# Optimization experiments

Measured on AMD Instinct MI355X. Metric: run time of the kernel, lower is better.

## Reference

```python
import jax, jax.numpy as jnp
import numpy as np

N_NODES = 50000
IN_DIM = 128
HIDDEN = 64
OUT_DIM = 3
HEADS1 = 4
NEG_SLOPE = 0.2
EPS = 1e-16


def _glorot(key, shape):
    fan_in, fan_out = shape[0], shape[-1]
    lim = (6.0 / (fan_in + fan_out)) ** 0.5
    return jax.random.uniform(key, shape, jnp.float32, -lim, lim)


def setup_inputs() -> dict:
    key = jax.random.key(0)
    ks = jax.random.split(key, 12)
    x = jax.random.normal(ks[0], (N_NODES, IN_DIM), jnp.float32)
    edge_index = jax.random.randint(ks[1], (2, 400000), 0, N_NODES, jnp.int64)
    # layer 1: GATConv(in=128, out=64, heads=4)
    W1 = _glorot(ks[2], (IN_DIM, HEADS1 * HIDDEN))
    att_src1 = _glorot(ks[3], (HEADS1, HIDDEN))
    att_dst1 = _glorot(ks[4], (HEADS1, HIDDEN))
    b1 = jnp.zeros((HEADS1 * HIDDEN,), jnp.float32)
    # layer 2: GATConv(in=256, out=64, heads=1)
    W2 = _glorot(ks[5], (HEADS1 * HIDDEN, HIDDEN))
    att_src2 = _glorot(ks[6], (1, HIDDEN))
    att_dst2 = _glorot(ks[7], (1, HIDDEN))
    b2 = jnp.zeros((HIDDEN,), jnp.float32)
    # output linear
    Wout = _glorot(ks[8], (HIDDEN, OUT_DIM))
    bout = jnp.zeros((OUT_DIM,), jnp.float32)
    return {"x": x, "edge_index": edge_index, "W1": W1, "att_src1": att_src1,
            "att_dst1": att_dst1, "b1": b1, "W2": W2, "att_src2": att_src2,
            "att_dst2": att_dst2, "b2": b2, "Wout": Wout, "bout": bout}


def gat_conv(x, src, dst, W, a_src, a_dst, b, n_nodes):
    H, C = a_src.shape
    h = (x @ W).reshape(n_nodes, H, C)            # [N,H,C]
    a_s = jnp.sum(h * a_src[None], axis=-1)        # [N,H]
    a_d = jnp.sum(h * a_dst[None], axis=-1)        # [N,H]
    e = jax.nn.leaky_relu(a_s[src] + a_d[dst], NEG_SLOPE)  # [E,H]
    # segment softmax over incoming edges of each dst node
    m = jax.ops.segment_max(e, dst, num_segments=n_nodes)
    ex = jnp.exp(e - m[dst])
    denom = jax.ops.segment_sum(ex, dst, num_segments=n_nodes)
    alpha = ex / (denom[dst] + EPS)                # [E,H]
    msg = h[src] * alpha[..., None]                # [E,H,C]
    out = jax.ops.segment_sum(msg, dst, num_segments=n_nodes)
    return out.reshape(n_nodes, H * C) + b


def reference(x, edge_index, W1, att_src1, att_dst1, b1, W2, att_src2, att_dst2, b2, Wout, bout):
    n = x.shape[0]
    loop = jnp.arange(n, dtype=edge_index.dtype)
    src = jnp.concatenate([edge_index[0], loop])   # add self loops (PyG default)
    dst = jnp.concatenate([edge_index[1], loop])
    h = gat_conv(x, src, dst, W1, att_src1, att_dst1, b1, n)
    h = jax.nn.elu(h)
    h = gat_conv(h, src, dst, W2, att_src2, att_dst2, b2, n)
    h = jax.nn.elu(h)
    return h @ Wout + bout
```

## Files before the change

kernel.cpp:

```cpp
#include <hip/hip_runtime.h>
#include <hip/hip_bf16.h>
#include <math.h>

#define N_NODES  50000
#define IN_DIM   128
#define HIDDEN   64
#define OUT_DIM  3
#define HEADS1   4
#define E_RAW    400000
#define E_TOT    450000
#define NEG_SLOPE 0.2f
#define N_CHUNKS 49
#define WPREP_BLOCKS 128
#define EB_SC ((E_TOT + 255) / 256)
#define MB_GE (N_NODES / 16)

typedef __attribute__((ext_vector_type(8))) short bf16x8;
typedef __attribute__((ext_vector_type(4))) float f32x4;

static __device__ __forceinline__ float bfu(unsigned short u) {
    return __uint_as_float(((unsigned)u) << 16);
}
static __device__ __forceinline__ unsigned short f2b_bits(float v) {
    __hip_bfloat16 b = __float2bfloat16(v);
    return *reinterpret_cast<unsigned short*>(&b);
}

static __device__ __forceinline__ void get_edge(const int* __restrict__ ei, int is64,
                                                int e, int& s, int& d) {
    if (e >= E_RAW) { s = d = e - E_RAW; return; }
    if (is64) { s = ei[2 * e]; d = ei[2 * E_RAW + 2 * e]; }
    else      { s = ei[e];     d = ei[E_RAW + e]; }
    s = min(max(s, 0), N_NODES - 1);
    d = min(max(d, 0), N_NODES - 1);
}

static __device__ __forceinline__ int block_is64(const int* __restrict__ ei,
                                                 int e, bool valid, int* nzbuf) {
    bool real = valid && (e < E_RAW);
    int hv = real ? ei[2 * e + 1] : 0;
    if (threadIdx.x == 0) *nzbuf = 0;
    __syncthreads();
    if (__any(hv != 0) && (threadIdx.x & 63) == 0) *nzbuf = 1;
    __syncthreads();
    return (*nzbuf == 0);
}

__global__ void wprep_count_kernel(const float* __restrict__ W1, __hip_bfloat16* __restrict__ W1T,
                                   const float* __restrict__ W2, __hip_bfloat16* __restrict__ W2T,
                                   const int* __restrict__ ei, int* __restrict__ deg) {
    __shared__ int nz;
    int bid = blockIdx.x;
    if (bid < WPREP_BLOCKS) {
        int i = bid * 256 + threadIdx.x;
        if (i < 256 * 128) {
            int n = i >> 7, k = i & 127;
            *((unsigned short*)W1T + i) = f2b_bits(W1[k * 256 + n]);
        }
        if (i < 64 * 256) {
            int n = i >> 8, k = i & 255;
            *((unsigned short*)W2T + i) = f2b_bits(W2[k * 64 + n]);
        }
        return;
    }
    int e = (bid - WPREP_BLOCKS) * 256 + threadIdx.x;
    bool valid = e < E_TOT;
    int is64 = block_is64(ei, e, valid, &nz);
    if (!valid) return;
    int s, d;
    get_edge(ei, is64, e, s, d);
    atomicAdd(&deg[d], 1);
}

__global__ void scan_fused_kernel(const int* __restrict__ deg, int* __restrict__ row_ptr,
                                  int* __restrict__ cursor) {
    __shared__ int wsum[4];
    __shared__ int sbase;
    const int bid = blockIdx.x, t = threadIdx.x, wv = t >> 6, ln = t & 63;
    int base = 0;
    const int ng = bid * 256;
    for (int g = t; g < ng; g += 256) {
        int4 d = ((const int4*)deg)[g];
        base += (d.x + d.y) + (d.z + d.w);
    }
    #pragma unroll
    for (int off = 1; off < 64; off <<= 1) base += __shfl_xor(base, off, 64);
    if (ln == 0) wsum[wv] = base;
    __syncthreads();
    if (t == 0) sbase = wsum[0] + wsum[1] + wsum[2] + wsum[3];
    __syncthreads();
    base = sbase;
    int g = bid * 256 + t;
    int4 d = (g < 12500) ? ((const int4*)deg)[g] : make_int4(0, 0, 0, 0);
    int p0 = d.x, p1 = p0 + d.y, p2 = p1 + d.z, p3 = p2 + d.w;
    int s = p3;
    #pragma unroll
    for (int off = 1; off < 64; off <<= 1) {
        int u = __shfl_up(s, off, 64);
        if (ln >= off) s += u;
    }
    if (ln == 63) wsum[wv] = s;
    __syncthreads();
    int wbase = base;
    #pragma unroll
    for (int w = 0; w < 4; w++) wbase += (w < wv) ? wsum[w] : 0;
    int ex = wbase + s - p3;
    if (g < 12500) {
        int i = g * 4;
        row_ptr[i + 1] = ex + p0; row_ptr[i + 2] = ex + p1;
        row_ptr[i + 3] = ex + p2; row_ptr[i + 4] = ex + p3;
        cursor[i]     = ex;       cursor[i + 1]  = ex + p0;
        cursor[i + 2] = ex + p1;  cursor[i + 3]  = ex + p2;
    }
    if (bid == 0 && t == 0) row_ptr[0] = 0;
}

__global__ void __launch_bounds__(256) scatter_gemm_l1_kernel(
        const int* __restrict__ ei,
        int* __restrict__ cursor, int* __restrict__ csr_src,
        const float* __restrict__ x, const __hip_bfloat16* __restrict__ W1T,
        const float* __restrict__ att_s, const float* __restrict__ att_d,
        __hip_bfloat16* __restrict__ h1,
        float* __restrict__ asb4, float* __restrict__ adb4) {
    __shared__ unsigned short As[16][136];
    __shared__ __attribute__((aligned(16))) unsigned short hT[16][264];
    __shared__ int nz;
    if (blockIdx.x < EB_SC) {
        int e = blockIdx.x * 256 + threadIdx.x;
        bool valid = e < E_TOT;
        int is64 = block_is64(ei, e, valid, &nz);
        if (!valid) return;
        int s, d;
        get_edge(ei, is64, e, s, d);
        int pos = atomicAdd(&cursor[d], 1);
        csr_src[pos] = s;
        return;
    }
    const int tid = threadIdx.x;
    const int wave = tid >> 6, lane = tid & 63;
    const int quad = lane >> 4, m = lane & 15;
    const int row0 = (blockIdx.x - EB_SC) * 16;
    {
        int r = tid >> 4, seg = tid & 15;
        const float* xa = x + (size_t)(row0 + r) * IN_DIM + seg * 8;
        float4 u = *(const float4*)xa;
        float4 v = *(const float4*)(xa + 4);
        ushort4 p0, p1;
        p0.x = f2b_bits(u.x); p0.y = f2b_bits(u.y); p0.z = f2b_bits(u.z); p0.w = f2b_bits(u.w);
        p1.x = f2b_bits(v.x); p1.y = f2b_bits(v.y); p1.z = f2b_bits(v.z); p1.w = f2b_bits(v.w);
        *(ushort4*)&As[r][seg * 8]     = p0;
        *(ushort4*)&As[r][seg * 8 + 4] = p1;
    }
    __syncthreads();
    const int n0w = wave * 64;
    f32x4 acc0 = {0.f, 0.f, 0.f, 0.f}, acc1 = acc0, acc2 = acc0, acc3 = acc0;
    #pragma unroll
    for (int k0 = 0; k0 < IN_DIM; k0 += 32) {
        int kk = k0 + quad * 8;
        bf16x8 a = *(const bf16x8*)&As[m][kk];
        bf16x8 b0 = *(const bf16x8*)(W1T + (size_t)(n0w +  0 + m) * IN_DIM + kk);
        bf16x8 b1 = *(const bf16x8*)(W1T + (size_t)(n0w + 16 + m) * IN_DIM + kk);
        bf16x8 b2 = *(const bf16x8*)(W1T + (size_t)(n0w + 32 + m) * IN_DIM + kk);
        bf16x8 b3 = *(const bf16x8*)(W1T + (size_t)(n0w + 48 + m) * IN_DIM + kk);
        acc0 = __builtin_amdgcn_mfma_f32_16x16x32_bf16(a, b0, acc0, 0, 0, 0);
        acc1 = __builtin_amdgcn_mfma_f32_16x16x32_bf16(a, b1, acc1, 0, 0, 0);
        acc2 = __builtin_amdgcn_mfma_f32_16x16x32_bf16(a, b2, acc2, 0, 0, 0);
        acc3 = __builtin_amdgcn_mfma_f32_16x16x32_bf16(a, b3, acc3, 0, 0, 0);
    }
    float ats0 = att_s[n0w +  0 + m], atd0 = att_d[n0w +  0 + m];
    float ats1 = att_s[n0w + 16 + m], atd1 = att_d[n0w + 16 + m];
    float ats2 = att_s[n0w + 32 + m], atd2 = att_d[n0w + 32 + m];
    float ats3 = att_s[n0w + 48 + m], atd3 = att_d[n0w + 48 + m];
    #pragma unroll
    for (int i = 0; i < 4; i++) {
        int r = quad * 4 + i;
        hT[r][n0w +  0 + m] = f2b_bits(acc0[i]);
        hT[r][n0w + 16 + m] = f2b_bits(acc1[i]);
        hT[r][n0w + 32 + m] = f2b_bits(acc2[i]);
        hT[r][n0w + 48 + m] = f2b_bits(acc3[i]);
        float ps = acc0[i] * ats0 + acc1[i] * ats1 + acc2[i] * ats2 + acc3[i] * ats3;
        float pd = acc0[i] * atd0 + acc1[i] * atd1 + acc2[i] * atd2 + acc3[i] * atd3;
        #pragma unroll
        for (int off = 1; off < 16; off <<= 1) {
            ps += __shfl_xor(ps, off, 16);
            pd += __shfl_xor(pd, off, 16);
        }
        if (m == 0) {
            asb4[(row0 + r) * 4 + wave] = ps;
            adb4[(row0 + r) * 4 + wave] = pd;
        }
    }
    __syncthreads();
    {
        unsigned short* hrow = (unsigned short*)h1;
        int r0 = tid >> 5, c0 = tid & 31;
        *(bf16x8*)(hrow + (size_t)(row0 + r0) * 256 + c0 * 8) = *(const bf16x8*)&hT[r0][c0 * 8];
        int S = tid + 256;
        int r1 = S >> 5, c1 = S & 31;
        *(bf16x8*)(hrow + (size_t)(row0 + r1) * 256 + c1 * 8) = *(const bf16x8*)&hT[r1][c1 * 8];
    }
}

__global__ void __launch_bounds__(1024, 8) gat_gather4_l2_kernel(
        const int* __restrict__ row_ptr, const int* __restrict__ csr_src,
        const float* __restrict__ asb4, const float* __restrict__ adb4,
        const __hip_bfloat16* __restrict__ h1, const float* __restrict__ bias,
        const __hip_bfloat16* __restrict__ W2T,
        const float* __restrict__ att_s, const float* __restrict__ att_d,
        __hip_bfloat16* __restrict__ h2,
        float* __restrict__ asb, float* __restrict__ adb) {
    __shared__ __attribute__((aligned(16))) unsigned short As[16][264];
    __shared__ __attribute__((aligned(16))) unsigned short hT2[16][72];
    __shared__ float sPS[4][16];
    __shared__ float sPD[4][16];
    const int tid = threadIdx.x;
    const int wave = tid >> 6, lane = tid & 63;
    const int row0 = blockIdx.x * 16;
    const int c    = lane & 31;
    const int slot = lane >> 5;
    const int head = c >> 3;
    const int eidx0 = lane >> 2;
    const int hh   = lane & 3;

    {
        const int n = row0 + wave;
        int b = row_ptr[n], e = row_ptr[n + 1];
        float adnh = adb4[n * 4 + hh];
        float acc[8];
        #pragma unroll
        for (int i = 0; i < 8; i++) acc[i] = 0.f;
        float l = 0.f;
        for (int c0 = b; c0 < e; c0 += 16) {
            int cnt = min(16, e - c0);
            int s_all = (lane < cnt) ? csr_src[c0 + lane] : 0;
            int sE = __shfl(s_all, eidx0, 64);
            float w_all = 0.f;
            if (eidx0 < cnt) {
                float v = asb4[sE * 4 + hh] + adnh;
                v = (v > 0.f) ? v : NEG_SLOPE * v;
                w_all = __expf(v);
            }
            #pragma unroll 2
            for (int k = 0; k < cnt; k += 2) {
                int eidx = k + slot;
                int s = __shfl(s_all, eidx, 64);
                float w = __shfl(w_all, eidx * 4 + head, 64);
                bf16x8 f = *(const bf16x8*)(h1 + (size_t)s * 256 + c * 8);
                l += w;
                #pragma unroll
                for (int i = 0; i < 8; i++)
                    acc[i] += w * bfu((unsigned short)f[i]);
            }
        }
        #pragma unroll
        for (int i = 0; i < 8; i++) acc[i] += __shfl_xor(acc[i], 32, 64);
        l += __shfl_xor(l, 32, 64);
        if (lane < 32) {
            float il = 1.f / (l + 1e-16f);
            float4 b0 = *(const float4*)(bias + c * 8);
            float4 b1 = *(const float4*)(bias + c * 8 + 4);
            float r[8];
            r[0] = acc[0] * il + b0.x; r[1] = acc[1] * il + b0.y;
            r[2] = acc[2] * il + b0.z; r[3] = acc[3] * il + b0.w;
            r[4] = acc[4] * il + b1.x; r[5] = acc[5] * il + b1.y;
            r[6] = acc[6] * il + b1.z; r[7] = acc[7] * il + b1.w;
            bf16x8 st;
            #pragma unroll
            for (int i = 0; i < 8; i++) {
                float v = (r[i] > 0.f) ? r[i] : expm1f(r[i]);
                st[i] = (short)f2b_bits(v);
            }
            *(bf16x8*)&As[wave][c * 8] = st;
        }
    }
    __syncthreads();

    if (wave < 4) {
        const int quad = lane >> 4, m = lane & 15;
        const int n0 = wave * 16;
        f32x4 acc = {0.f, 0.f, 0.f, 0.f};
        #pragma unroll
        for (int k0 = 0; k0 < 256; k0 += 32) {
            int kk = k0 + quad * 8;
            bf16x8 a = *(const bf16x8*)&As[m][kk];
            bf16x8 bfr = *(const bf16x8*)(W2T + (size_t)(n0 + m) * 256 + kk);
            acc = __builtin_amdgcn_mfma_f32_16x16x32_bf16(a, bfr, acc, 0, 0, 0);
        }
        float ats = att_s[n0 + m], atd = att_d[n0 + m];
        #pragma unroll
        for (int i = 0; i < 4; i++) {
            int r = quad * 4 + i;
            hT2[r][n0 + m] = f2b_bits(acc[i]);
            float ps = acc[i] * ats;
            float pd = acc[i] * atd;
            #pragma unroll
            for (int off = 1; off < 16; off <<= 1) {
                ps += __shfl_xor(ps, off, 16);
                pd += __shfl_xor(pd, off, 16);
            }
            if (m == 0) {
                sPS[wave][r] = ps;
                sPD[wave][r] = pd;
            }
        }
    }
    __syncthreads();
    if (tid < 128) {
        int r = tid >> 3, cs = tid & 7;
        *(bf16x8*)((unsigned short*)h2 + (size_t)(row0 + r) * 64 + cs * 8) =
            *(const bf16x8*)&hT2[r][cs * 8];
    }
    if (tid < 16) {
        float ps = sPS[0][tid] + sPS[1][tid] + sPS[2][tid] + sPS[3][tid];
        float pd = sPD[0][tid] + sPD[1][tid] + sPD[2][tid] + sPD[3][tid];
        asb[row0 + tid] = ps;
        adb[row0 + tid] = pd;
    }
}

__global__ void __launch_bounds__(256) gat_gather1_out_kernel(
        const int* __restrict__ row_ptr, const int* __restrict__ csr_src,
        const float* __restrict__ asb, const float* __restrict__ adb,
        const __hip_bfloat16* __restrict__ h2, const float* __restrict__ bias,
        const float* __restrict__ Wout, const float* __restrict__ bout,
        float* __restrict__ out) {
    int wave = threadIdx.x >> 6;
    int lane = threadIdx.x & 63;
    int n = blockIdx.x * 4 + wave;
    if (n >= N_NODES) return;
    int b = row_ptr[n], e = row_ptr[n + 1];
    const int c    = lane & 7;
    const int slot = lane >> 3;
    float adn = adb[n];
    float acc[8];
    #pragma unroll
    for (int i = 0; i < 8; i++) acc[i] = 0.f;
    float l = 0.f;
    for (int c0 = b; c0 < e; c0 += 64) {
        int cnt = min(64, e - c0);
        int s_all = (lane < cnt) ? csr_src[c0 + lane] : 0;
        float w_all = 0.f;
        if (lane < cnt) {
            float v = asb[s_all] + adn;
            v = (v > 0.f) ? v : NEG_SLOPE * v;
            w_all = __expf(v);
        }
        #pragma unroll 2
        for (int k = 0; k < cnt; k += 8) {
            int eidx = k + slot;
            int s = __shfl(s_all, eidx, 64);
            float w = __shfl(w_all, eidx, 64);
            bf16x8 f = *(const bf16x8*)(h2 + (size_t)s * 64 + c * 8);
            l += w;
            #pragma unroll
            for (int i = 0; i < 8; i++)
                acc[i] += w * bfu((unsigned short)f[i]);
        }
    }
    #pragma unroll
    for (int off = 8; off < 64; off <<= 1) {
        #pragma unroll
        for (int i = 0; i < 8; i++) acc[i] += __shfl_xor(acc[i], off, 64);
        l += __shfl_xor(l, off, 64);
    }
    float il = 1.f / (l + 1e-16f);
    float4 b0 = *(const float4*)(bias + c * 8);
    float4 b1 = *(const float4*)(bias + c * 8 + 4);
    float v[8];
    v[0] = acc[0] * il + b0.x; v[1] = acc[1] * il + b0.y;
    v[2] = acc[2] * il + b0.z; v[3] = acc[3] * il + b0.w;
    v[4] = acc[4] * il + b1.x; v[5] = acc[5] * il + b1.y;
    v[6] = acc[6] * il + b1.z; v[7] = acc[7] * il + b1.w;
    #pragma unroll
    for (int i = 0; i < 8; i++) v[i] = (v[i] > 0.f) ? v[i] : expm1f(v[i]);
    const float* wp = Wout + c * 24;
    float o0 = 0.f, o1 = 0.f, o2 = 0.f;
    #pragma unroll
    for (int i = 0; i < 8; i++) {
        o0 += v[i] * wp[i * 3 + 0];
        o1 += v[i] * wp[i * 3 + 1];
        o2 += v[i] * wp[i * 3 + 2];
    }
    #pragma unroll
    for (int off = 1; off < 8; off <<= 1) {
        o0 += __shfl_xor(o0, off, 64);
        o1 += __shfl_xor(o1, off, 64);
        o2 += __shfl_xor(o2, off, 64);
    }
    if (lane == 0) {
        out[n * OUT_DIM + 0] = o0 + bout[0];
        out[n * OUT_DIM + 1] = o1 + bout[1];
        out[n * OUT_DIM + 2] = o2 + bout[2];
    }
}

extern "C" void kernel_launch(void* const* d_in, const int* in_sizes, int n_in,
                              void* d_out, int out_size, void* d_ws, size_t ws_size,
                              hipStream_t stream) {
    const float* x    = (const float*)d_in[0];
    const int*   ei   = (const int*)d_in[1];
    const float* W1   = (const float*)d_in[2];
    const float* as1  = (const float*)d_in[3];
    const float* ad1  = (const float*)d_in[4];
    const float* b1   = (const float*)d_in[5];
    const float* W2   = (const float*)d_in[6];
    const float* as2  = (const float*)d_in[7];
    const float* ad2  = (const float*)d_in[8];
    const float* b2v  = (const float*)d_in[9];
    const float* Wout = (const float*)d_in[10];
    const float* bout = (const float*)d_in[11];
    float* out = (float*)d_out;

    float* ws    = (float*)d_ws;
    float* asb4  = ws + 16;
    float* adb4  = asb4 + (size_t)N_NODES * 4;
    float* asb1  = adb4 + (size_t)N_NODES * 4;
    float* adb1  = asb1 + N_NODES;
    __hip_bfloat16* h1     = (__hip_bfloat16*)(adb1 + N_NODES);
    __hip_bfloat16* h2     = (__hip_bfloat16*)(h1 + (size_t)N_NODES * 256);
    __hip_bfloat16* W1T    = (__hip_bfloat16*)(h2 + (size_t)N_NODES * 64);
    __hip_bfloat16* W2T    = W1T + 256 * 128;
    int* deg     = (int*)(W2T + 64 * 256);
    int* row_ptr = deg + N_NODES;
    int* cursor  = row_ptr + N_NODES + 16;
    int* csr_src = cursor + N_NODES;

    const int EB = EB_SC;
    const int AB = (N_NODES + 3) / 4;

    hipMemsetAsync(deg, 0, (size_t)N_NODES * sizeof(int), stream);
    wprep_count_kernel<<<WPREP_BLOCKS + EB, 256, 0, stream>>>(W1, W1T, W2, W2T, ei, deg);
    scan_fused_kernel<<<N_CHUNKS, 256, 0, stream>>>(deg, row_ptr, cursor);

    scatter_gemm_l1_kernel<<<EB + MB_GE, 256, 0, stream>>>(ei, cursor, csr_src,
                                                           x, W1T, as1, ad1, h1, asb4, adb4);

    gat_gather4_l2_kernel<<<MB_GE, 1024, 0, stream>>>(row_ptr, csr_src, asb4, adb4, h1, b1,
                                                      W2T, as2, ad2, h2, asb1, adb1);

    gat_gather1_out_kernel<<<AB, 256, 0, stream>>>(row_ptr, csr_src, asb1, adb1, h2,
                                                   b2v, Wout, bout, out);
}
```

Baseline: 260.9 us.

## Fuse GAT pipeline into single persistent cooperative kernel with grid syncs

Replaces the memset plus five separate kernel launches with one cooperative persistent kernel that runs each stage (weight prep, degree count, scan, CSR scatter with layer-1 GEMM, layer-2 gather/GEMM, final gather/output) in grid-stride loops separated by grid.sync. The int64 detection becomes a single vote in block 0 written to a flag, instead of a per-block vote. The aim is to remove launch overhead and inter-kernel gaps. In exchange, every stage is limited to the grid size chosen from occupancy, and the layer-2 stage shrinks from 1024-thread blocks to 256-thread blocks, which may lower parallelism and lengthen the serialized phases.

Result: slower. 726.7 us (+178.6%).

```diff
diff --git a/kernel.cpp b/kernel.cpp
--- a/kernel.cpp
+++ b/kernel.cpp
@@ -1,6 +1,9 @@
 #include <hip/hip_runtime.h>
+#include <hip/hip_cooperative_groups.h>
 #include <hip/hip_bf16.h>
 #include <math.h>
+
+namespace cg = cooperative_groups;
 
 #define N_NODES  50000
 #define IN_DIM   128
@@ -11,9 +14,9 @@
 #define E_TOT    450000
 #define NEG_SLOPE 0.2f
 #define N_CHUNKS 49
-#define WPREP_BLOCKS 128
 #define EB_SC ((E_TOT + 255) / 256)
 #define MB_GE (N_NODES / 16)
+#define AB_G  ((N_NODES + 3) / 4)
 
 typedef __attribute__((ext_vector_type(8))) short bf16x8;
 typedef __attribute__((ext_vector_type(4))) float f32x4;
@@ -35,262 +38,261 @@
     d = min(max(d, 0), N_NODES - 1);
 }
 
-static __device__ __forceinline__ int block_is64(const int* __restrict__ ei,
-                                                 int e, bool valid, int* nzbuf) {
-    bool real = valid && (e < E_RAW);
-    int hv = real ? ei[2 * e + 1] : 0;
-    if (threadIdx.x == 0) *nzbuf = 0;
-    __syncthreads();
-    if (__any(hv != 0) && (threadIdx.x & 63) == 0) *nzbuf = 1;
-    __syncthreads();
-    return (*nzbuf == 0);
-}
-
-__global__ void wprep_count_kernel(const float* __restrict__ W1, __hip_bfloat16* __restrict__ W1T,
-                                   const float* __restrict__ W2, __hip_bfloat16* __restrict__ W2T,
-                                   const int* __restrict__ ei, int* __restrict__ deg) {
-    __shared__ int nz;
-    int bid = blockIdx.x;
-    if (bid < WPREP_BLOCKS) {
-        int i = bid * 256 + threadIdx.x;
-        if (i < 256 * 128) {
-            int n = i >> 7, k = i & 127;
-            *((unsigned short*)W1T + i) = f2b_bits(W1[k * 256 + n]);
-        }
-        if (i < 64 * 256) {
-            int n = i >> 8, k = i & 255;
-            *((unsigned short*)W2T + i) = f2b_bits(W2[k * 64 + n]);
-        }
-        return;
-    }
-    int e = (bid - WPREP_BLOCKS) * 256 + threadIdx.x;
-    bool valid = e < E_TOT;
-    int is64 = block_is64(ei, e, valid, &nz);
-    if (!valid) return;
-    int s, d;
-    get_edge(ei, is64, e, s, d);
-    atomicAdd(&deg[d], 1);
-}
-
-__global__ void scan_fused_kernel(const int* __restrict__ deg, int* __restrict__ row_ptr,
-                                  int* __restrict__ cursor) {
+struct MegaArgs {
+    const float* x; const int* ei;
+    const float* W1; const float* as1; const float* ad1; const float* b1;
+    const float* W2; const float* as2; const float* ad2; const float* b2v;
+    const float* Wout; const float* bout;
+    float* out;
+    int* flag;
+    float *asb4, *adb4, *asb1, *adb1;
+    __hip_bfloat16 *h1, *eluagg, *h2, *W1T, *W2T;
+    int *deg, *row_ptr, *cursor, *csr_src;
+};
+
+__global__ void __launch_bounds__(256) gat_mega_kernel(MegaArgs a) {
+    cg::grid_group grid = cg::this_grid();
+    const int tid = threadIdx.x;
+    const int nb = gridDim.x;
+    const int gsz = nb * 256;
+    const int gid0 = blockIdx.x * 256 + tid;
+    const int wave = tid >> 6, lane = tid & 63;
+
+    __shared__ unsigned short As[16][136];
+    __shared__ __attribute__((aligned(16))) unsigned short hT[16][264];
+    __shared__ float sPS[4][16];
+    __shared__ float sPD[4][16];
+    __shared__ int ivote;
     __shared__ int wsum[4];
     __shared__ int sbase;
-    const int bid = blockIdx.x, t = threadIdx.x, wv = t >> 6, ln = t & 63;
-    int base = 0;
-    const int ng = bid * 256;
-    for (int g = t; g < ng; g += 256) {
-        int4 d = ((const int4*)deg)[g];
-        base += (d.x + d.y) + (d.z + d.w);
-    }
-    #pragma unroll
-    for (int off = 1; off < 64; off <<= 1) base += __shfl_xor(base, off, 64);
-    if (ln == 0) wsum[wv] = base;
-    __syncthreads();
-    if (t == 0) sbase = wsum[0] + wsum[1] + wsum[2] + wsum[3];
-    __syncthreads();
-    base = sbase;
-    int g = bid * 256 + t;
-    int4 d = (g < 12500) ? ((const int4*)deg)[g] : make_int4(0, 0, 0, 0);
-    int p0 = d.x, p1 = p0 + d.y, p2 = p1 + d.z, p3 = p2 + d.w;
-    int s = p3;
-    #pragma unroll
-    for (int off = 1; off < 64; off <<= 1) {
-        int u = __shfl_up(s, off, 64);
-        if (ln >= off) s += u;
-    }
-    if (ln == 63) wsum[wv] = s;
-    __syncthreads();
-    int wbase = base;
-    #pragma unroll
-    for (int w = 0; w < 4; w++) wbase += (w < wv) ? wsum[w] : 0;
-    int ex = wbase + s - p3;
-    if (g < 12500) {
-        int i = g * 4;
-        row_ptr[i + 1] = ex + p0; row_ptr[i + 2] = ex + p1;
-        row_ptr[i + 3] = ex + p2; row_ptr[i + 4] = ex + p3;
-        cursor[i]     = ex;       cursor[i + 1]  = ex + p0;
-        cursor[i + 2] = ex + p1;  cursor[i + 3]  = ex + p2;
-    }
-    if (bid == 0 && t == 0) row_ptr[0] = 0;
-}
-
-__global__ void __launch_bounds__(256) scatter_gemm_l1_kernel(
-        const int* __restrict__ ei,
-        int* __restrict__ cursor, int* __restrict__ csr_src,
-        const float* __restrict__ x, const __hip_bfloat16* __restrict__ W1T,
-        const float* __restrict__ att_s, const float* __restrict__ att_d,
-        __hip_bfloat16* __restrict__ h1,
-        float* __restrict__ asb4, float* __restrict__ adb4) {
-    __shared__ unsigned short As[16][136];
-    __shared__ __attribute__((aligned(16))) unsigned short hT[16][264];
-    __shared__ int nz;
-    if (blockIdx.x < EB_SC) {
-        int e = blockIdx.x * 256 + threadIdx.x;
-        bool valid = e < E_TOT;
-        int is64 = block_is64(ei, e, valid, &nz);
-        if (!valid) return;
+
+    for (int i = gid0; i < N_NODES; i += gsz) a.deg[i] = 0;
+    for (int i = gid0; i < 256 * 128; i += gsz) {
+        int n = i >> 7, k = i & 127;
+        *((unsigned short*)a.W1T + i) = f2b_bits(a.W1[k * 256 + n]);
+    }
+    for (int i = gid0; i < 64 * 256; i += gsz) {
+        int n = i >> 8, k = i & 255;
+        *((unsigned short*)a.W2T + i) = f2b_bits(a.W2[k * 64 + n]);
+    }
+    if (blockIdx.x == 0) {
+        int nzv = 0;
+        #pragma unroll 4
+        for (int t = 0; t < 32; t++) {
+            int i = t * 256 + tid;
+            nzv |= a.ei[2 * i + 1];
+        }
+        if (tid == 0) ivote = 0;
+        __syncthreads();
+        if (__any(nzv != 0) && (tid & 63) == 0) ivote = 1;
+        __syncthreads();
+        if (tid == 0) a.flag[0] = (ivote == 0) ? 1 : 0;
+    }
+    grid.sync();
+
+    const int is64 = a.flag[0];
+    for (int e = gid0; e < E_TOT; e += gsz) {
         int s, d;
-        get_edge(ei, is64, e, s, d);
-        int pos = atomicAdd(&cursor[d], 1);
-        csr_src[pos] = s;
-        return;
-    }
-    const int tid = threadIdx.x;
-    const int wave = tid >> 6, lane = tid & 63;
-    const int quad = lane >> 4, m = lane & 15;
-    const int row0 = (blockIdx.x - EB_SC) * 16;
+        get_edge(a.ei, is64, e, s, d);
+        atomicAdd(&a.deg[d], 1);
+    }
+    grid.sync();
+
+    if (blockIdx.x < N_CHUNKS) {
+        const int bid = blockIdx.x, wv = wave, ln = lane;
+        int base = 0;
+        const int ng = bid * 256;
+        for (int g = tid; g < ng; g += 256) {
+            int4 d = ((const int4*)a.deg)[g];
+            base += (d.x + d.y) + (d.z + d.w);
+        }
+        #pragma unroll
+        for (int off = 1; off < 64; off <<= 1) base += __shfl_xor(base, off, 64);
+        if (ln == 0) wsum[wv] = base;
+        __syncthreads();
+        if (tid == 0) sbase = wsum[0] + wsum[1] + wsum[2] + wsum[3];
+        __syncthreads();
+        base = sbase;
+        int g = bid * 256 + tid;
+        int4 d = (g < 12500) ? ((const int4*)a.deg)[g] : make_int4(0, 0, 0, 0);
+        int p0 = d.x, p1 = p0 + d.y, p2 = p1 + d.z, p3 = p2 + d.w;
+        int s = p3;
+        #pragma unroll
+        for (int off = 1; off < 64; off <<= 1) {
+            int u = __shfl_up(s, off, 64);
+            if (ln >= off) s += u;
+        }
+        if (ln == 63) wsum[wv] = s;
+        __syncthreads();
+        int wbase = base;
+        #pragma unroll
+        for (int w = 0; w < 4; w++) wbase += (w < wv) ? wsum[w] : 0;
+        int ex = wbase + s - p3;
+        if (g < 12500) {
+            int i = g * 4;
+            a.row_ptr[i + 1] = ex + p0; a.row_ptr[i + 2] = ex + p1;
+            a.row_ptr[i + 3] = ex + p2; a.row_ptr[i + 4] = ex + p3;
+            a.cursor[i]     = ex;       a.cursor[i + 1]  = ex + p0;
+            a.cursor[i + 2] = ex + p1;  a.cursor[i + 3]  = ex + p2;
+        }
+        if (bid == 0 && tid == 0) a.row_ptr[0] = 0;
+    }
+    grid.sync();
+
+    for (int vb = blockIdx.x; vb < EB_SC + MB_GE; vb += nb) {
+        if (vb < EB_SC) {
+            int e = vb * 256 + tid;
+            if (e < E_TOT) {
+                int s, d;
+                get_edge(a.ei, is64, e, s, d);
+                int pos = atomicAdd(&a.cursor[d], 1);
+                a.csr_src[pos] = s;
+            }
+        } else {
+            const int quad = lane >> 4, m = lane & 15;
+            const int row0 = (vb - EB_SC) * 16;
+            {
+                int r = tid >> 4, seg = tid & 15;
+                const float* xa = a.x + (size_t)(row0 + r) * IN_DIM + seg * 8;
+                float4 u = *(const float4*)xa;
+                float4 v = *(const float4*)(xa + 4);
+                ushort4 p0, p1;
+                p0.x = f2b_bits(u.x); p0.y = f2b_bits(u.y); p0.z = f2b_bits(u.z); p0.w = f2b_bits(u.w);
+                p1.x = f2b_bits(v.x); p1.y = f2b_bits(v.y); p1.z = f2b_bits(v.z); p1.w = f2b_bits(v.w);
+                *(ushort4*)&As[r][seg * 8]     = p0;
+                *(ushort4*)&As[r][seg * 8 + 4] = p1;
+            }
+            __syncthreads();
+            const int n0w = wave * 64;
+            f32x4 acc0 = {0.f, 0.f, 0.f, 0.f}, acc1 = acc0, acc2 = acc0, acc3 = acc0;
+            #pragma unroll
+            for (int k0 = 0; k0 < IN_DIM; k0 += 32) {
+                int kk = k0 + quad * 8;
+                bf16x8 av = *(const bf16x8*)&As[m][kk];
+                bf16x8 b0 = *(const bf16x8*)(a.W1T + (size_t)(n0w +  0 + m) * IN_DIM + kk);
+                bf16x8 b1 = *(const bf16x8*)(a.W1T + (size_t)(n0w + 16 + m) * IN_DIM + kk);
+                bf16x8 b2 = *(const bf16x8*)(a.W1T + (size_t)(n0w + 32 + m) * IN_DIM + kk);
+                bf16x8 b3 = *(const bf16x8*)(a.W1T + (size_t)(n0w + 48 + m) * IN_DIM + kk);
+                acc0 = __builtin_amdgcn_mfma_f32_16x16x32_bf16(av, b0, acc0, 0, 0, 0);
+                acc1 = __builtin_amdgcn_mfma_f32_16x16x32_bf16(av, b1, acc1, 0, 0, 0);
+                acc2 = __builtin_amdgcn_mfma_f32_16x16x32_bf16(av, b2, acc2, 0, 0, 0);
+                acc3 = __builtin_amdgcn_mfma_f32_16x16x32_bf16(av, b3, acc3, 0, 0, 0);
+            }
+            float ats0 = a.as1[n0w +  0 + m], atd0 = a.ad1[n0w +  0 + m];
+            float ats1 = a.as1[n0w + 16 + m], atd1 = a.ad1[n0w + 16 + m];
+            float ats2 = a.as1[n0w + 32 + m], atd2 = a.ad1[n0w + 32 + m];
+            float ats3 = a.as1[n0w + 48 + m], atd3 = a.ad1[n0w + 48 + m];
+            #pragma unroll
+            for (int i = 0; i < 4; i++) {
+                int r = quad * 4 + i;
+                hT[r][n0w +  0 + m] = f2b_bits(acc0[i]);
+                hT[r][n0w + 16 + m] = f2b_bits(acc1[i]);
+                hT[r][n0w + 32 + m] = f2b_bits(acc2[i]);
+                hT[r][n0w + 48 + m] = f2b_bits(acc3[i]);
+                float ps = acc0[i] * ats0 + acc1[i] * ats1 + acc2[i] * ats2 + acc3[i] * ats3;
+                float pd = acc0[i] * atd0 + acc1[i] * atd1 + acc2[i] * atd2 + acc3[i] * atd3;
+                #pragma unroll
+                for (int off = 1; off < 16; off <<= 1) {
+                    ps += __shfl_xor(ps, off, 16);
+                    pd += __shfl_xor(pd, off, 16);
+                }
+                if (m == 0) {
+                    a.asb4[(row0 + r) * 4 + wave] = ps;
+                    a.adb4[(row0 + r) * 4 + wave] = pd;
+                }
+            }
+            __syncthreads();
+            {
+                unsigned short* hrow = (unsigned short*)a.h1;
+                int r0 = tid >> 5, c0 = tid & 31;
+                *(bf16x8*)(hrow + (size_t)(row0 + r0) * 256 + c0 * 8) = *(const bf16x8*)&hT[r0][c0 * 8];
+                int S = tid + 256;
+                int r1 = S >> 5, c1 = S & 31;
+                *(bf16x8*)(hrow + (size_t)(row0 + r1) * 256 + c1 * 8) = *(const bf16x8*)&hT[r1][c1 * 8];
+            }
+            __syncthreads();
+        }
+    }
+    grid.sync();
+
     {
-        int r = tid >> 4, seg = tid & 15;
-        const float* xa = x + (size_t)(row0 + r) * IN_DIM + seg * 8;
-        float4 u = *(const float4*)xa;
-        float4 v = *(const float4*)(xa + 4);
-        ushort4 p0, p1;
-        p0.x = f2b_bits(u.x); p0.y = f2b_bits(u.y); p0.z = f2b_bits(u.z); p0.w = f2b_bits(u.w);
-        p1.x = f2b_bits(v.x); p1.y = f2b_bits(v.y); p1.z = f2b_bits(v.z); p1.w = f2b_bits(v.w);
-        *(ushort4*)&As[r][seg * 8]     = p0;
-        *(ushort4*)&As[r][seg * 8 + 4] = p1;
-    }
-    __syncthreads();
-    const int n0w = wave * 64;
-    f32x4 acc0 = {0.f, 0.f, 0.f, 0.f}, acc1 = acc0, acc2 = acc0, acc3 = acc0;
-    #pragma unroll
-    for (int k0 = 0; k0 < IN_DIM; k0 += 32) {
-        int kk = k0 + quad * 8;
-        bf16x8 a = *(const bf16x8*)&As[m][kk];
-        bf16x8 b0 = *(const bf16x8*)(W1T + (size_t)(n0w +  0 + m) * IN_DIM + kk);
-        bf16x8 b1 = *(const bf16x8*)(W1T + (size_t)(n0w + 16 + m) * IN_DIM + kk);
-        bf16x8 b2 = *(const bf16x8*)(W1T + (size_t)(n0w + 32 + m) * IN_DIM + kk);
-        bf16x8 b3 = *(const bf16x8*)(W1T + (size_t)(n0w + 48 + m) * IN_DIM + kk);
-        acc0 = __builtin_amdgcn_mfma_f32_16x16x32_bf16(a, b0, acc0, 0, 0, 0);
-        acc1 = __builtin_amdgcn_mfma_f32_16x16x32_bf16(a, b1, acc1, 0, 0, 0);
-        acc2 = __builtin_amdgcn_mfma_f32_16x16x32_bf16(a, b2, acc2, 0, 0, 0);
-        acc3 = __builtin_amdgcn_mfma_f32_16x16x32_bf16(a, b3, acc3, 0, 0, 0);
-    }
-    float ats0 = att_s[n0w +  0 + m], atd0 = att_d[n0w +  0 + m];
-    float ats1 = att_s[n0w + 16 + m], atd1 = att_d[n0w + 16 + m];
-    float ats2 = att_s[n0w + 32 + m], atd2 = att_d[n0w + 32 + m];
-    float ats3 = att_s[n0w + 48 + m], atd3 = att_d[n0w + 48 + m];
-    #pragma unroll
-    for (int i = 0; i < 4; i++) {
-        int r = quad * 4 + i;
-        hT[r][n0w +  0 + m] = f2b_bits(acc0[i]);
-        hT[r][n0w + 16 + m] = f2b_bits(acc1[i]);
-        hT[r][n0w + 32 + m] = f2b_bits(acc2[i]);
-        hT[r][n0w + 48 + m] = f2b_bits(acc3[i]);
-        float ps = acc0[i] * ats0 + acc1[i] * ats1 + acc2[i] * ats2 + acc3[i] * ats3;
-        float pd = acc0[i] * atd0 + acc1[i] * atd1 + acc2[i] * atd2 + acc3[i] * atd3;
-        #pragma unroll
-        for (int off = 1; off < 16; off <<= 1) {
-            ps += __shfl_xor(ps, off, 16);
-            pd += __shfl_xor(pd, off, 16);
-        }
-        if (m == 0) {
-            asb4[(row0 + r) * 4 + wave] = ps;
-            adb4[(row0 + r) * 4 + wave] = pd;
-        }
-    }
-    __syncthreads();
-    {
-        unsigned short* hrow = (unsigned short*)h1;
-        int r0 = tid >> 5, c0 = tid & 31;
-        *(bf16x8*)(hrow + (size_t)(row0 + r0) * 256 + c0 * 8) = *(const bf16x8*)&hT[r0][c0 * 8];
-        int S = tid + 256;
-        int r1 = S >> 5, c1 = S & 31;
-        *(bf16x8*)(hrow + (size_t)(row0 + r1) * 256 + c1 * 8) = *(const bf16x8*)&hT[r1][c1 * 8];
-    }
-}
-
-__global__ void __launch_bounds__(1024, 8) gat_gather4_l2_kernel(
-        const int* __restrict__ row_ptr, const int* __restrict__ csr_src,
-        const float* __restrict__ asb4, const float* __restrict__ adb4,
-        const __hip_bfloat16* __restrict__ h1, const float* __restrict__ bias,
-        const __hip_bfloat16* __restrict__ W2T,
-        const float* __restrict__ att_s, const float* __restrict__ att_d,
-        __hip_bfloat16* __restrict__ h2,
-        float* __restrict__ asb, float* __restrict__ adb) {
-    __shared__ __attribute__((aligned(16))) unsigned short As[16][264];
-    __shared__ __attribute__((aligned(16))) unsigned short hT2[16][72];
-    __shared__ float sPS[4][16];
-    __shared__ float sPD[4][16];
-    const int tid = threadIdx.x;
-    const int wave = tid >> 6, lane = tid & 63;
-    const int row0 = blockIdx.x * 16;
-    const int c    = lane & 31;
-    const int slot = lane >> 5;
-    const int head = c >> 3;
-    const int eidx0 = lane >> 2;
-    const int hh   = lane & 3;
-
-    {
-        const int n = row0 + wave;
-        int b = row_ptr[n], e = row_ptr[n + 1];
-        float adnh = adb4[n * 4 + hh];
-        float acc[8];
-        #pragma unroll
-        for (int i = 0; i < 8; i++) acc[i] = 0.f;
-        float l = 0.f;
-        for (int c0 = b; c0 < e; c0 += 16) {
-            int cnt = min(16, e - c0);
-            int s_all = (lane < cnt) ? csr_src[c0 + lane] : 0;
-            int sE = __shfl(s_all, eidx0, 64);
-            float w_all = 0.f;
-            if (eidx0 < cnt) {
-                float v = asb4[sE * 4 + hh] + adnh;
-                v = (v > 0.f) ? v : NEG_SLOPE * v;
-                w_all = __expf(v);
-            }
-            #pragma unroll 2
-            for (int k = 0; k < cnt; k += 2) {
-                int eidx = k + slot;
-                int s = __shfl(s_all, eidx, 64);
-                float w = __shfl(w_all, eidx * 4 + head, 64);
-                bf16x8 f = *(const bf16x8*)(h1 + (size_t)s * 256 + c * 8);
-                l += w;
+        const int c    = lane & 31;
+        const int slot = lane >> 5;
+        const int head = c >> 3;
+        const int eidx0 = lane >> 2;
+        const int hh   = lane & 3;
+        for (int vb = blockIdx.x; vb < AB_G; vb += nb) {
+            const int n = vb * 4 + wave;
+            int b = a.row_ptr[n], en = a.row_ptr[n + 1];
+            float adnh = a.adb4[n * 4 + hh];
+            float acc[8];
+            #pragma unroll
+            for (int i = 0; i < 8; i++) acc[i] = 0.f;
+            float l = 0.f;
+            for (int c0 = b; c0 < en; c0 += 16) {
+                int cnt = min(16, en - c0);
+                int s_all = (lane < cnt) ? a.csr_src[c0 + lane] : 0;
+                int sE = __shfl(s_all, eidx0, 64);
+                float w_all = 0.f;
+                if (eidx0 < cnt) {
+                    float v = a.asb4[sE * 4 + hh] + adnh;
+                    v = (v > 0.f) ? v : NEG_SLOPE * v;
+                    w_all = __expf(v);
+                }
+                #pragma unroll 2
+                for (int k = 0; k < cnt; k += 2) {
+                    int eidx = k + slot;
+                    int s = __shfl(s_all, eidx, 64);
+                    float w = __shfl(w_all, eidx * 4 + head, 64);
+                    bf16x8 f = *(const bf16x8*)(a.h1 + (size_t)s * 256 + c * 8);
+                    l += w;
+                    #pragma unroll
+                    for (int i = 0; i < 8; i++)
+                        acc[i] += w * bfu((unsigned short)f[i]);
+                }
+            }
+            #pragma unroll
+            for (int i = 0; i < 8; i++) acc[i] += __shfl_xor(acc[i], 32, 64);
+            l += __shfl_xor(l, 32, 64);
+            if (lane < 32) {
+                float il = 1.f / (l + 1e-16f);
+                float4 b0 = *(const float4*)(a.b1 + c * 8);
+                float4 b1 = *(const float4*)(a.b1 + c * 8 + 4);
+                float r[8];
+                r[0] = acc[0] * il + b0.x; r[1] = acc[1] * il + b0.y;
+                r[2] = acc[2] * il + b0.z; r[3] = acc[3] * il + b0.w;
+                r[4] = acc[4] * il + b1.x; r[5] = acc[5] * il + b1.y;
+                r[6] = acc[6] * il + b1.z; r[7] = acc[7] * il + b1.w;
+                bf16x8 st;
                 #pragma unroll
-                for (int i = 0; i < 8; i++)
-                    acc[i] += w * bfu((unsigned short)f[i]);
-            }
-        }
-        #pragma unroll
-        for (int i = 0; i < 8; i++) acc[i] += __shfl_xor(acc[i], 32, 64);
-        l += __shfl_xor(l, 32, 64);
-        if (lane < 32) {
-            float il = 1.f / (l + 1e-16f);
-            float4 b0 = *(const float4*)(bias + c * 8);
-            float4 b1 = *(const float4*)(bias + c * 8 + 4);
-            float r[8];
-            r[0] = acc[0] * il + b0.x; r[1] = acc[1] * il + b0.y;
-            r[2] = acc[2] * il + b0.z; r[3] = acc[3] * il + b0.w;
-            r[4] = acc[4] * il + b1.x; r[5] = acc[5] * il + b1.y;
-            r[6] = acc[6] * il + b1.z; r[7] = acc[7] * il + b1.w;
-            bf16x8 st;
-            #pragma unroll
-            for (int i = 0; i < 8; i++) {
-                float v = (r[i] > 0.f) ? r[i] : expm1f(r[i]);
-                st[i] = (short)f2b_bits(v);
-            }
-            *(bf16x8*)&As[wave][c * 8] = st;
-        }
-    }
-    __syncthreads();
-
-    if (wave < 4) {
+                for (int i = 0; i < 8; i++) {
+                    float v = (r[i] > 0.f) ? r[i] : expm1f(r[i]);
+                    st[i] = (short)f2b_bits(v);
+                }
+                *(bf16x8*)(a.eluagg + (size_t)n * 256 + c * 8) = st;
+            }
+        }
+    }
+    grid.sync();
+
+    for (int vb = blockIdx.x; vb < MB_GE; vb += nb) {
         const int quad = lane >> 4, m = lane & 15;
+        const int row0 = vb * 16;
         const int n0 = wave * 16;
         f32x4 acc = {0.f, 0.f, 0.f, 0.f};
         #pragma unroll
         for (int k0 = 0; k0 < 256; k0 += 32) {
             int kk = k0 + quad * 8;
-            bf16x8 a = *(const bf16x8*)&As[m][kk];
-            bf16x8 bfr = *(const bf16x8*)(W2T + (size_t)(n0 + m) * 256 + kk);
-            acc = __builtin_amdgcn_mfma_f32_16x16x32_bf16(a, bfr, acc, 0, 0, 0);
-        }
-        float ats = att_s[n0 + m], atd = att_d[n0 + m];
+            bf16x8 av = *(const bf16x8*)(a.eluagg + (size_t)(row0 + m) * 256 + kk);
+            bf16x8 bv = *(const bf16x8*)(a.W2T + (size_t)(n0 + m) * 256 + kk);
+            acc = __builtin_amdgcn_mfma_f32_16x16x32_bf16(av, bv, acc, 0, 0, 0);
+        }
+        float ats = a.as2[n0 + m], atd = a.ad2[n0 + m];
+        unsigned short* outp = (unsigned short*)a.h2;
         #pragma unroll
         for (int i = 0; i < 4; i++) {
-            int r = quad * 4 + i;
-            hT2[r][n0 + m] = f2b_bits(acc[i]);
+            int grow = row0 + quad * 4 + i;
+            outp[(size_t)grow * 64 + n0 + m] = f2b_bits(acc[i]);
             float ps = acc[i] * ats;
             float pd = acc[i] * atd;
             #pragma unroll
@@ -299,145 +301,136 @@
                 pd += __shfl_xor(pd, off, 16);
             }
             if (m == 0) {
-                sPS[wave][r] = ps;
-                sPD[wave][r] = pd;
-            }
-        }
-    }
-    __syncthreads();
-    if (tid < 128) {
-        int r = tid >> 3, cs = tid & 7;
-        *(bf16x8*)((unsigned short*)h2 + (size_t)(row0 + r) * 64 + cs * 8) =
-            *(const bf16x8*)&hT2[r][cs * 8];
-    }
-    if (tid < 16) {
-        float ps = sPS[0][tid] + sPS[1][tid] + sPS[2][tid] + sPS[3][tid];
-        float pd = sPD[0][tid] + sPD[1][tid] + sPD[2][tid] + sPD[3][tid];
-        asb[row0 + tid] = ps;
-        adb[row0 + tid] = pd;
-    }
-}
-
-__global__ void __launch_bounds__(256) gat_gather1_out_kernel(
-        const int* __restrict__ row_ptr, const int* __restrict__ csr_src,
-        const float* __restrict__ asb, const float* __restrict__ adb,
-        const __hip_bfloat16* __restrict__ h2, const float* __restrict__ bias,
-        const float* __restrict__ Wout, const float* __restrict__ bout,
-        float* __restrict__ out) {
-    int wave = threadIdx.x >> 6;
-    int lane = threadIdx.x & 63;
-    int n = blockIdx.x * 4 + wave;
-    if (n >= N_NODES) return;
-    int b = row_ptr[n], e = row_ptr[n + 1];
-    const int c    = lane & 7;
-    const int slot = lane >> 3;
-    float adn = adb[n];
-    float acc[8];
-    #pragma unroll
-    for (int i = 0; i < 8; i++) acc[i] = 0.f;
-    float l = 0.f;
-    for (int c0 = b; c0 < e; c0 += 64) {
-        int cnt = min(64, e - c0);
-        int s_all = (lane < cnt) ? csr_src[c0 + lane] : 0;
-        float w_all = 0.f;
-        if (lane < cnt) {
-            float v = asb[s_all] + adn;
-            v = (v > 0.f) ? v : NEG_SLOPE * v;
-            w_all = __expf(v);
-        }
-        #pragma unroll 2
-        for (int k = 0; k < cnt; k += 8) {
-            int eidx = k + slot;
-            int s = __shfl(s_all, eidx, 64);
-            float w = __shfl(w_all, eidx, 64);
-            bf16x8 f = *(const bf16x8*)(h2 + (size_t)s * 64 + c * 8);
-            l += w;
-            #pragma unroll
-            for (int i = 0; i < 8; i++)
-                acc[i] += w * bfu((unsigned short)f[i]);
-        }
-    }
-    #pragma unroll
-    for (int off = 8; off < 64; off <<= 1) {
-        #pragma unroll
-        for (int i = 0; i < 8; i++) acc[i] += __shfl_xor(acc[i], off, 64);
-        l += __shfl_xor(l, off, 64);
-    }
-    float il = 1.f / (l + 1e-16f);
-    float4 b0 = *(const float4*)(bias + c * 8);
-    float4 b1 = *(const float4*)(bias + c * 8 + 4);
-    float v[8];
-    v[0] = acc[0] * il + b0.x; v[1] = acc[1] * il + b0.y;
-    v[2] = acc[2] * il + b0.z; v[3] = acc[3] * il + b0.w;
-    v[4] = acc[4] * il + b1.x; v[5] = acc[5] * il + b1.y;
-    v[6] = acc[6] * il + b1.z; v[7] = acc[7] * il + b1.w;
-    #pragma unroll
-    for (int i = 0; i < 8; i++) v[i] = (v[i] > 0.f) ? v[i] : expm1f(v[i]);
-    const float* wp = Wout + c * 24;
-    float o0 = 0.f, o1 = 0.f, o2 = 0.f;
-    #pragma unroll
-    for (int i = 0; i < 8; i++) {
-        o0 += v[i] * wp[i * 3 + 0];
-        o1 += v[i] * wp[i * 3 + 1];
-        o2 += v[i] * wp[i * 3 + 2];
-    }
-    #pragma unroll
-    for (int off = 1; off < 8; off <<= 1) {
-        o0 += __shfl_xor(o0, off, 64);
-        o1 += __shfl_xor(o1, off, 64);
-        o2 += __shfl_xor(o2, off, 64);
-    }
-    if (lane == 0) {
-        out[n * OUT_DIM + 0] = o0 + bout[0];
-        out[n * OUT_DIM + 1] = o1 + bout[1];
-        out[n * OUT_DIM + 2] = o2 + bout[2];
+                sPS[wave][quad * 4 + i] = ps;
+                sPD[wave][quad * 4 + i] = pd;
+            }
+        }
+        __syncthreads();
+        if (tid < 16) {
+            float ps = sPS[0][tid] + sPS[1][tid] + sPS[2][tid] + sPS[3][tid];
+            float pd = sPD[0][tid] + sPD[1][tid] + sPD[2][tid] + sPD[3][tid];
+            a.asb1[row0 + tid] = ps;
+            a.adb1[row0 + tid] = pd;
+        }
+        __syncthreads();
+    }
+    grid.sync();
+
+    {
+        const int c    = lane & 7;
+        const int slot = lane >> 3;
+        for (int vb = blockIdx.x; vb < AB_G; vb += nb) {
+            const int n = vb * 4 + wave;
+            int b = a.row_ptr[n], en = a.row_ptr[n + 1];
+            float adn = a.adb1[n];
+            float acc[8];
+            #pragma unroll
+            for (int i = 0; i < 8; i++) acc[i] = 0.f;
+            float l = 0.f;
+            for (int c0 = b; c0 < en; c0 += 64) {
+                int cnt = min(64, en - c0);
+                int s_all = (lane < cnt) ? a.csr_src[c0 + lane] : 0;
+                float w_all = 0.f;
+                if (lane < cnt) {
+                    float v = a.asb1[s_all] + adn;
+                    v = (v > 0.f) ? v : NEG_SLOPE * v;
+                    w_all = __expf(v);
+                }
+                #pragma unroll 2
+                for (int k = 0; k < cnt; k += 8) {
+                    int eidx = k + slot;
+                    int s = __shfl(s_all, eidx, 64);
+                    float w = __shfl(w_all, eidx, 64);
+                    bf16x8 f = *(const bf16x8*)(a.h2 + (size_t)s * 64 + c * 8);
+                    l += w;
+                    #pragma unroll
+                    for (int i = 0; i < 8; i++)
+                        acc[i] += w * bfu((unsigned short)f[i]);
+                }
+            }
+            #pragma unroll
+            for (int off = 8; off < 64; off <<= 1) {
+                #pragma unroll
+                for (int i = 0; i < 8; i++) acc[i] += __shfl_xor(acc[i], off, 64);
+                l += __shfl_xor(l, off, 64);
+            }
+            float il = 1.f / (l + 1e-16f);
+            float4 b0 = *(const float4*)(a.b2v + c * 8);
+            float4 b1 = *(const float4*)(a.b2v + c * 8 + 4);
+            float v[8];
+            v[0] = acc[0] * il + b0.x; v[1] = acc[1] * il + b0.y;
+            v[2] = acc[2] * il + b0.z; v[3] = acc[3] * il + b0.w;
+            v[4] = acc[4] * il + b1.x; v[5] = acc[5] * il + b1.y;
+            v[6] = acc[6] * il + b1.z; v[7] = acc[7] * il + b1.w;
+            #pragma unroll
+            for (int i = 0; i < 8; i++) v[i] = (v[i] > 0.f) ? v[i] : expm1f(v[i]);
+            const float* wp = a.Wout + c * 24;
+            float o0 = 0.f, o1 = 0.f, o2 = 0.f;
+            #pragma unroll
+            for (int i = 0; i < 8; i++) {
+                o0 += v[i] * wp[i * 3 + 0];
+                o1 += v[i] * wp[i * 3 + 1];
+                o2 += v[i] * wp[i * 3 + 2];
+            }
+            #pragma unroll
+            for (int off = 1; off < 8; off <<= 1) {
+                o0 += __shfl_xor(o0, off, 64);
+                o1 += __shfl_xor(o1, off, 64);
+                o2 += __shfl_xor(o2, off, 64);
+            }
+            if (lane == 0) {
+                a.out[n * OUT_DIM + 0] = o0 + a.bout[0];
+                a.out[n * OUT_DIM + 1] = o1 + a.bout[1];
+                a.out[n * OUT_DIM + 2] = o2 + a.bout[2];
+            }
+        }
     }
 }
 
 extern "C" void kernel_launch(void* const* d_in, const int* in_sizes, int n_in,
                               void* d_out, int out_size, void* d_ws, size_t ws_size,
                               hipStream_t stream) {
-    const float* x    = (const float*)d_in[0];
-    const int*   ei   = (const int*)d_in[1];
-    const float* W1   = (const float*)d_in[2];
-    const float* as1  = (const float*)d_in[3];
-    const float* ad1  = (const float*)d_in[4];
-    const float* b1   = (const float*)d_in[5];
-    const float* W2   = (const float*)d_in[6];
-    const float* as2  = (const float*)d_in[7];
-    const float* ad2  = (const float*)d_in[8];
-    const float* b2v  = (const float*)d_in[9];
-    const float* Wout = (const float*)d_in[10];
-    const float* bout = (const float*)d_in[11];
-    float* out = (float*)d_out;
-
-    float* ws    = (float*)d_ws;
-    float* asb4  = ws + 16;
-    float* adb4  = asb4 + (size_t)N_NODES * 4;
-    float* asb1  = adb4 + (size_t)N_NODES * 4;
-    float* adb1  = asb1 + N_NODES;
-    __hip_bfloat16* h1     = (__hip_bfloat16*)(adb1 + N_NODES);
-    __hip_bfloat16* h2     = (__hip_bfloat16*)(h1 + (size_t)N_NODES * 256);
-    __hip_bfloat16* W1T    = (__hip_bfloat16*)(h2 + (size_t)N_NODES * 64);
-    __hip_bfloat16* W2T    = W1T + 256 * 128;
-    int* deg     = (int*)(W2T + 64 * 256);
-    int* row_ptr = deg + N_NODES;
-    int* cursor  = row_ptr + N_NODES + 16;
-    int* csr_src = cursor + N_NODES;
-
-    const int EB = EB_SC;
-    const int AB = (N_NODES + 3) / 4;
-
-    hipMemsetAsync(deg, 0, (size_t)N_NODES * sizeof(int), stream);
-    wprep_count_kernel<<<WPREP_BLOCKS + EB, 256, 0, stream>>>(W1, W1T, W2, W2T, ei, deg);
-    scan_fused_kernel<<<N_CHUNKS, 256, 0, stream>>>(deg, row_ptr, cursor);
-
-    scatter_gemm_l1_kernel<<<EB + MB_GE, 256, 0, stream>>>(ei, cursor, csr_src,
-                                                           x, W1T, as1, ad1, h1, asb4, adb4);
-
-    gat_gather4_l2_kernel<<<MB_GE, 1024, 0, stream>>>(row_ptr, csr_src, asb4, adb4, h1, b1,
-                                                      W2T, as2, ad2, h2, asb1, adb1);
-
-    gat_gather1_out_kernel<<<AB, 256, 0, stream>>>(row_ptr, csr_src, asb1, adb1, h2,
-                                                   b2v, Wout, bout, out);
+    MegaArgs a;
+    a.x    = (const float*)d_in[0];
+    a.ei   = (const int*)d_in[1];
+    a.W1   = (const float*)d_in[2];
+    a.as1  = (const float*)d_in[3];
+    a.ad1  = (const float*)d_in[4];
+    a.b1   = (const float*)d_in[5];
+    a.W2   = (const float*)d_in[6];
+    a.as2  = (const float*)d_in[7];
+    a.ad2  = (const float*)d_in[8];
+    a.b2v  = (const float*)d_in[9];
+    a.Wout = (const float*)d_in[10];
+    a.bout = (const float*)d_in[11];
+    a.out  = (float*)d_out;
+
+    float* ws = (float*)d_ws;
+    a.flag  = (int*)ws;
+    a.asb4  = ws + 16;
+    a.adb4  = a.asb4 + (size_t)N_NODES * 4;
+    a.asb1  = a.adb4 + (size_t)N_NODES * 4;
+    a.adb1  = a.asb1 + N_NODES;
+    a.h1     = (__hip_bfloat16*)(a.adb1 + N_NODES);
+    a.eluagg = a.h1 + (size_t)N_NODES * 256;
+    a.h2     = a.eluagg + (size_t)N_NODES * 256;
+    a.W1T    = a.h2 + (size_t)N_NODES * 64;
+    a.W2T    = a.W1T + 256 * 128;
+    a.deg     = (int*)(a.W2T + 64 * 256);
+    a.row_ptr = a.deg + N_NODES;
+    a.cursor  = a.row_ptr + N_NODES + 16;
+    a.csr_src = a.cursor + N_NODES;
+
+    static int g_grid = 0;
+    if (g_grid == 0) {
+        int perCU = 0;
+        hipError_t err = hipOccupancyMaxActiveBlocksPerMultiprocessor(&perCU, gat_mega_kernel, 256, 0);
+        if (err != hipSuccess || perCU <= 0) perCU = 4;
+        long g = (long)perCU * 256;
+        if (g > 2048) g = 2048;
+        if (g < 64) g = 64;
+        g_grid = (int)g;
+    }
+    void* kp[] = { (void*)&a };
+    hipLaunchCooperativeKernel(gat_mega_kernel, dim3(g_grid), dim3(256), kp, 0, stream);
 }
```
